# Performance work log

Hardware: AMD Instinct MI355X
Metric: run time of the kernel (lower is better)

The kernel has to match this reference:

```python
import jax, jax.numpy as jnp
import numpy as np

B, H, S, D = 2, 16, 2048, 64

def setup_inputs() -> dict:
    key = jax.random.key(0)
    kq, kk, kv, km = jax.random.split(key, 4)
    Query = jax.random.normal(kq, (B, H, S, D), dtype=jnp.float32)
    Key = jax.random.normal(kk, (B, H, S, D), dtype=jnp.float32)
    Value = jax.random.normal(kv, (B, H, S, D), dtype=jnp.float32)
    attention_mask = jax.random.randint(km, (B, 1, S, S), 0, 2).astype(jnp.bool_)
    return {"Query": Query, "Key": Key, "Value": Value,
            "attention_mask": attention_mask, "dim_key": D}

def reference(Query, Key, Value, attention_mask, dim_key):
    # scores: [B,H,S,S]
    scale = 1.0 / np.sqrt(dim_key).astype(np.float32)
    scores = jnp.einsum('bhqd,bhkd->bhqk', Query, Key) * scale
    scores = jnp.where(attention_mask, jnp.float32(-1e9), scores)
    attention = jax.nn.softmax(scores, axis=-1)
    context = jnp.einsum('bhqk,bhkd->bhqd', attention, Value)
    return (context, attention)
```

## Files before the change

### kernel.cpp

```cpp
#include <hip/hip_runtime.h>
#include <hip/hip_bf16.h>


#define S_LEN 2048
#define D_DIM 64
#define LOG2E 1.44269504088896340736f

typedef __attribute__((ext_vector_type(8))) short bf16x8;
typedef __attribute__((ext_vector_type(4))) float f32x4;

__device__ __forceinline__ short f2bs(float f) {
    union { __hip_bfloat16 h; short s; } u;
    u.h = __float2bfloat16(f);
    return u.s;
}

__device__ __forceinline__ unsigned int f2bs2(float x, float y) {
    float2 t = make_float2(x, y);
    union { __hip_bfloat162 h; unsigned int u; } u;
    u.h = __float22bfloat162_rn(t);
    return u.u;
}

__device__ __forceinline__ bf16x8 cvt8(float4 a, float4 b) {
    union { bf16x8 v; unsigned int w[4]; } u;
    u.w[0] = f2bs2(a.x, a.y);
    u.w[1] = f2bs2(a.z, a.w);
    u.w[2] = f2bs2(b.x, b.y);
    u.w[3] = f2bs2(b.z, b.w);
    return u.v;
}

__global__ __launch_bounds__(512, 4) void sdpa_kernel(
    const float* __restrict__ Q, const float* __restrict__ K,
    const float* __restrict__ V, const int* __restrict__ Mask,
    float* __restrict__ Ctx, float* __restrict__ Attn)
{
    __shared__ __attribute__((aligned(16))) short Kt[64 * 72];
    __shared__ __attribute__((aligned(16))) short Vt[64 * 72];
    __shared__ __attribute__((aligned(16))) short Pt[8 * 16 * 72];

    const int tid  = threadIdx.x;
    const int wave = tid >> 6;
    const int lane = tid & 63;
    const int quad = lane >> 4;
    const int l16  = lane & 15;

    const int bid = blockIdx.x;
    const int bh  = bid >> 4;
    const int qt  = bid & 15;
    const int b   = bh >> 4;

    const size_t sd_off = (size_t)bh * S_LEN * D_DIM;
    const float* Qbh = Q + sd_off;
    const float* Kbh = K + sd_off;
    const float* Vbh = V + sd_off;
    const int*   Mb  = Mask + (size_t)b * S_LEN * S_LEN;
    float* Cbh = Ctx + sd_off;
    float* Abh = Attn + (size_t)bh * S_LEN * S_LEN;

    const int qw = qt * 128 + wave * 16;

    bf16x8 qfrag[2];
    {
        const int qrow = qw + l16;
        #pragma unroll
        for (int kc = 0; kc < 2; ++kc) {
            const float* qp = Qbh + (size_t)qrow * D_DIM + kc * 32 + quad * 8;
            float4 a = *(const float4*)qp;
            float4 c = *(const float4*)(qp + 4);
            a.x *= 0.125f; a.y *= 0.125f; a.z *= 0.125f; a.w *= 0.125f;
            c.x *= 0.125f; c.y *= 0.125f; c.z *= 0.125f; c.w *= 0.125f;
            qfrag[kc] = cvt8(a, c);
        }
    }

    const int skey = tid >> 3;
    const int sd   = (tid & 7) * 8;

    float lacc[4] = {0.f, 0.f, 0.f, 0.f};

    for (int kt = 0; kt < 32; ++kt) {
        const int k0 = kt * 64;
        __syncthreads();
        {
            const float* kp = Kbh + (size_t)(k0 + skey) * D_DIM + sd;
            float4 a = *(const float4*)kp;
            float4 c = *(const float4*)(kp + 4);
            *(bf16x8*)&Kt[skey * 72 + sd] = cvt8(a, c);
        }
        __syncthreads();

        #pragma unroll
        for (int cc = 0; cc < 4; ++cc) {
            f32x4 acc = {0.f, 0.f, 0.f, 0.f};
            const int keyl = cc * 16 + l16;
            bf16x8 b0 = *(const bf16x8*)&Kt[keyl * 72 + quad * 8];
            bf16x8 b1 = *(const bf16x8*)&Kt[keyl * 72 + 32 + quad * 8];
            acc = __builtin_amdgcn_mfma_f32_16x16x32_bf16(qfrag[0], b0, acc, 0, 0, 0);
            acc = __builtin_amdgcn_mfma_f32_16x16x32_bf16(qfrag[1], b1, acc, 0, 0, 0);
            const int col = k0 + keyl;
            const int* mp = Mb + (size_t)(qw + quad * 4) * S_LEN + col;
            #pragma unroll
            for (int r = 0; r < 4; ++r) {
                int m = mp[(size_t)r * S_LEN];
                float p = m ? 0.f : exp2f(acc[r] * LOG2E);
                lacc[r] += p;
            }
        }
    }

    #pragma unroll
    for (int off = 1; off < 16; off <<= 1) {
        #pragma unroll
        for (int r = 0; r < 4; ++r)
            lacc[r] += __shfl_xor(lacc[r], off, 64);
    }
    float inv_l[4];
    #pragma unroll
    for (int r = 0; r < 4; ++r) inv_l[r] = 1.0f / lacc[r];

    f32x4 cacc[4];
    #pragma unroll
    for (int dc = 0; dc < 4; ++dc) cacc[dc] = (f32x4){0.f, 0.f, 0.f, 0.f};
    short* Pw = &Pt[wave * 16 * 72];

    for (int kt = 0; kt < 32; ++kt) {
        const int k0 = kt * 64;
        __syncthreads();
        {
            const float* kp = Kbh + (size_t)(k0 + skey) * D_DIM + sd;
            float4 a = *(const float4*)kp;
            float4 c = *(const float4*)(kp + 4);
            *(bf16x8*)&Kt[skey * 72 + sd] = cvt8(a, c);
            const float* vp = Vbh + (size_t)(k0 + skey) * D_DIM + sd;
            float4 va = *(const float4*)vp;
            float4 vb = *(const float4*)(vp + 4);
            float vv[8] = {va.x, va.y, va.z, va.w, vb.x, vb.y, vb.z, vb.w};
            #pragma unroll
            for (int i = 0; i < 8; ++i)
                Vt[(sd + i) * 72 + skey] = f2bs(vv[i]);
        }
        __syncthreads();

        #pragma unroll
        for (int cc = 0; cc < 4; ++cc) {
            f32x4 acc = {0.f, 0.f, 0.f, 0.f};
            const int keyl = cc * 16 + l16;
            bf16x8 b0 = *(const bf16x8*)&Kt[keyl * 72 + quad * 8];
            bf16x8 b1 = *(const bf16x8*)&Kt[keyl * 72 + 32 + quad * 8];
            acc = __builtin_amdgcn_mfma_f32_16x16x32_bf16(qfrag[0], b0, acc, 0, 0, 0);
            acc = __builtin_amdgcn_mfma_f32_16x16x32_bf16(qfrag[1], b1, acc, 0, 0, 0);
            const int col = k0 + keyl;
            const int* mp = Mb + (size_t)(qw + quad * 4) * S_LEN + col;
            float* ap = Abh + (size_t)(qw + quad * 4) * S_LEN + col;
            #pragma unroll
            for (int r = 0; r < 4; ++r) {
                int m = mp[(size_t)r * S_LEN];
                float p = m ? 0.f : exp2f(acc[r] * LOG2E);
                __builtin_nontemporal_store(p * inv_l[r], ap + (size_t)r * S_LEN);
                Pw[(quad * 4 + r) * 72 + keyl] = f2bs(p);
            }
        }

        #pragma unroll
        for (int kc = 0; kc < 2; ++kc) {
            bf16x8 af = *(const bf16x8*)&Pw[l16 * 72 + kc * 32 + quad * 8];
            #pragma unroll
            for (int dc = 0; dc < 4; ++dc) {
                bf16x8 bf = *(const bf16x8*)&Vt[(dc * 16 + l16) * 72 + kc * 32 + quad * 8];
                cacc[dc] = __builtin_amdgcn_mfma_f32_16x16x32_bf16(af, bf, cacc[dc], 0, 0, 0);
            }
        }
    }

    #pragma unroll
    for (int dc = 0; dc < 4; ++dc) {
        #pragma unroll
        for (int r = 0; r < 4; ++r) {
            Cbh[(size_t)(qw + quad * 4 + r) * D_DIM + dc * 16 + l16] =
                cacc[dc][r] * inv_l[r];
        }
    }
}

extern "C" void kernel_launch(void* const* d_in, const int* in_sizes, int n_in,
                              void* d_out, int out_size, void* d_ws, size_t ws_size,
                              hipStream_t stream) {
    const float* Q    = (const float*)d_in[0];
    const float* K    = (const float*)d_in[1];
    const float* V    = (const float*)d_in[2];
    const int*   Mask = (const int*)d_in[3];

    float* Ctx  = (float*)d_out;
    float* Attn = (float*)d_out + (size_t)2 * 16 * 2048 * 64;

    sdpa_kernel<<<dim3(512), dim3(512), 0, stream>>>(Q, K, V, Mask, Ctx, Attn);
}
```

Measured before the change: 760.8 us.

## Pre-convert K/V to bf16, bit-pack mask, use direct global-to-LDS loads

Adds a prep kernel that converts K and V to bf16 once, writing V pre-transposed, plus a kernel that packs the int mask into 64-bit bitmasks with ballot. The main kernel then loads tiles with global_load_lds into XOR-swizzled LDS, folds log2e into the Q scale, and uses native exp2. It also switches to 256-thread blocks of 64 queries with a head-grouped block order. This removes repeated per-block fp32 K/V conversion and the heavy int mask reads, in exchange for two extra launches and workspace traffic.

```diff
diff --git a/kernel.cpp b/kernel.cpp
--- a/kernel.cpp
+++ b/kernel.cpp
@@ -8,37 +8,93 @@
 
 typedef __attribute__((ext_vector_type(8))) short bf16x8;
 typedef __attribute__((ext_vector_type(4))) float f32x4;
-
+typedef unsigned long long u64;
+
+__device__ __forceinline__ unsigned int f2bs2(float x, float y) {
+    union { __hip_bfloat162 h; unsigned int u; } u;
+    u.h = __float22bfloat162_rn(make_float2(x, y));
+    return u.u;
+}
 __device__ __forceinline__ short f2bs(float f) {
     union { __hip_bfloat16 h; short s; } u;
     u.h = __float2bfloat16(f);
     return u.s;
 }
-
-__device__ __forceinline__ unsigned int f2bs2(float x, float y) {
-    float2 t = make_float2(x, y);
-    union { __hip_bfloat162 h; unsigned int u; } u;
-    u.h = __float22bfloat162_rn(t);
-    return u.u;
-}
-
 __device__ __forceinline__ bf16x8 cvt8(float4 a, float4 b) {
     union { bf16x8 v; unsigned int w[4]; } u;
-    u.w[0] = f2bs2(a.x, a.y);
-    u.w[1] = f2bs2(a.z, a.w);
-    u.w[2] = f2bs2(b.x, b.y);
-    u.w[3] = f2bs2(b.z, b.w);
+    u.w[0] = f2bs2(a.x, a.y); u.w[1] = f2bs2(a.z, a.w);
+    u.w[2] = f2bs2(b.x, b.y); u.w[3] = f2bs2(b.z, b.w);
     return u.v;
 }
 
-__global__ __launch_bounds__(512, 4) void sdpa_kernel(
-    const float* __restrict__ Q, const float* __restrict__ K,
-    const float* __restrict__ V, const int* __restrict__ Mask,
+__device__ __forceinline__ void gl2lds16(const short* g, short* l) {
+    __builtin_amdgcn_global_load_lds(
+        (const __attribute__((address_space(1))) unsigned int*)g,
+        (__attribute__((address_space(3))) unsigned int*)l, 16, 0, 0);
+}
+
+__global__ __launch_bounds__(256) void prep_kv(const float* __restrict__ K,
+                                               const float* __restrict__ V,
+                                               short* __restrict__ Kb,
+                                               short* __restrict__ Vtb) {
+    __shared__ short T[64 * 80];
+    const int bh = blockIdx.x >> 5;
+    const int kt = blockIdx.x & 31;
+    const int k0 = kt * 64;
+    const int t  = threadIdx.x;
+    const int row = t >> 2;
+    const int cq  = (t & 3) * 16;
+
+    const size_t base = (size_t)bh * S_LEN * D_DIM;
+    {
+        const float* kp = K + base + (size_t)(k0 + row) * D_DIM + cq;
+        float4 a = ((const float4*)kp)[0], b = ((const float4*)kp)[1],
+               c = ((const float4*)kp)[2], d = ((const float4*)kp)[3];
+        short* op = Kb + base + (size_t)(k0 + row) * D_DIM + cq;
+        *(bf16x8*)op       = cvt8(a, b);
+        *(bf16x8*)(op + 8) = cvt8(c, d);
+    }
+    {
+        const float* vp = V + base + (size_t)(k0 + row) * D_DIM + cq;
+        float4 a = ((const float4*)vp)[0], b = ((const float4*)vp)[1],
+               c = ((const float4*)vp)[2], d = ((const float4*)vp)[3];
+        float vv[16] = {a.x,a.y,a.z,a.w, b.x,b.y,b.z,b.w,
+                        c.x,c.y,c.z,c.w, d.x,d.y,d.z,d.w};
+        #pragma unroll
+        for (int i = 0; i < 16; ++i)
+            T[(cq + i) * 80 + row] = f2bs(vv[i]);
+    }
+    __syncthreads();
+    {
+        const int d  = t >> 2;
+        const int kc = (t & 3) * 16;
+        short* op = Vtb + (size_t)bh * D_DIM * S_LEN + (size_t)d * S_LEN + k0 + kc;
+        *(bf16x8*)op       = *(const bf16x8*)&T[d * 80 + kc];
+        *(bf16x8*)(op + 8) = *(const bf16x8*)&T[d * 80 + kc + 8];
+    }
+}
+
+__global__ __launch_bounds__(256) void mask_pack(const int* __restrict__ M,
+                                                 u64* __restrict__ Mp) {
+    const int lane = threadIdx.x & 63;
+    const int wid  = (blockIdx.x * 256 + threadIdx.x) >> 6;
+    const int nwaves = gridDim.x * 4;
+    const int nwords = 2 * S_LEN * (S_LEN / 64);
+    for (int w = wid; w < nwords; w += nwaves) {
+        int v = M[(size_t)w * 64 + lane];
+        u64 bits = __ballot(v != 0);
+        if (lane == 0) Mp[w] = bits;
+    }
+}
+
+__global__ __launch_bounds__(256, 4) void sdpa_main(
+    const float* __restrict__ Q, const short* __restrict__ Kb,
+    const short* __restrict__ Vtb, const u64* __restrict__ Mp,
     float* __restrict__ Ctx, float* __restrict__ Attn)
 {
-    __shared__ __attribute__((aligned(16))) short Kt[64 * 72];
-    __shared__ __attribute__((aligned(16))) short Vt[64 * 72];
-    __shared__ __attribute__((aligned(16))) short Pt[8 * 16 * 72];
+    __shared__ short Kt[64 * 64];
+    __shared__ short Vt[64 * 64];
+    __shared__ short Pt[4 * 16 * 80];
 
     const int tid  = threadIdx.x;
     const int wave = tid >> 6;
@@ -47,74 +103,68 @@
     const int l16  = lane & 15;
 
     const int bid = blockIdx.x;
-    const int bh  = bid >> 4;
-    const int qt  = bid & 15;
+    const int bh  = ((bid >> 8) << 3) | (bid & 7);
+    const int qt  = (bid >> 3) & 31;
     const int b   = bh >> 4;
+    const int qw  = qt * 64 + wave * 16;
 
     const size_t sd_off = (size_t)bh * S_LEN * D_DIM;
     const float* Qbh = Q + sd_off;
-    const float* Kbh = K + sd_off;
-    const float* Vbh = V + sd_off;
-    const int*   Mb  = Mask + (size_t)b * S_LEN * S_LEN;
+    const short* Kbh = Kb + sd_off;
+    const short* Vbh = Vtb + (size_t)bh * D_DIM * S_LEN;
     float* Cbh = Ctx + sd_off;
     float* Abh = Attn + (size_t)bh * S_LEN * S_LEN;
 
-    const int qw = qt * 128 + wave * 16;
-
     bf16x8 qfrag[2];
     {
         const int qrow = qw + l16;
+        const float s = 0.125f * LOG2E;
         #pragma unroll
         for (int kc = 0; kc < 2; ++kc) {
             const float* qp = Qbh + (size_t)qrow * D_DIM + kc * 32 + quad * 8;
-            float4 a = *(const float4*)qp;
-            float4 c = *(const float4*)(qp + 4);
-            a.x *= 0.125f; a.y *= 0.125f; a.z *= 0.125f; a.w *= 0.125f;
-            c.x *= 0.125f; c.y *= 0.125f; c.z *= 0.125f; c.w *= 0.125f;
+            float4 a = ((const float4*)qp)[0], c = ((const float4*)qp)[1];
+            a.x*=s; a.y*=s; a.z*=s; a.w*=s; c.x*=s; c.y*=s; c.z*=s; c.w*=s;
             qfrag[kc] = cvt8(a, c);
         }
     }
 
-    const int skey = tid >> 3;
-    const int sd   = (tid & 7) * 8;
+    const int mrow0 = (b * S_LEN + qw + quad * 4) * (S_LEN / 64);
 
     float lacc[4] = {0.f, 0.f, 0.f, 0.f};
-
     for (int kt = 0; kt < 32; ++kt) {
         const int k0 = kt * 64;
         __syncthreads();
-        {
-            const float* kp = Kbh + (size_t)(k0 + skey) * D_DIM + sd;
-            float4 a = *(const float4*)kp;
-            float4 c = *(const float4*)(kp + 4);
-            *(bf16x8*)&Kt[skey * 72 + sd] = cvt8(a, c);
-        }
-        __syncthreads();
-
+        #pragma unroll
+        for (int rd = 0; rd < 2; ++rd) {
+            const int m = tid + rd * 256;
+            const int row = m >> 3, sc = m & 7, c = sc ^ (row & 7);
+            gl2lds16(Kbh + (size_t)(k0 + row) * D_DIM + c * 8, &Kt[m * 8]);
+        }
+        __syncthreads();
+        u64 mw[4];
+        #pragma unroll
+        for (int r = 0; r < 4; ++r) mw[r] = Mp[mrow0 + r * 32 + kt];
         #pragma unroll
         for (int cc = 0; cc < 4; ++cc) {
+            const int keyl = cc * 16 + l16;
             f32x4 acc = {0.f, 0.f, 0.f, 0.f};
-            const int keyl = cc * 16 + l16;
-            bf16x8 b0 = *(const bf16x8*)&Kt[keyl * 72 + quad * 8];
-            bf16x8 b1 = *(const bf16x8*)&Kt[keyl * 72 + 32 + quad * 8];
-            acc = __builtin_amdgcn_mfma_f32_16x16x32_bf16(qfrag[0], b0, acc, 0, 0, 0);
-            acc = __builtin_amdgcn_mfma_f32_16x16x32_bf16(qfrag[1], b1, acc, 0, 0, 0);
-            const int col = k0 + keyl;
-            const int* mp = Mb + (size_t)(qw + quad * 4) * S_LEN + col;
+            #pragma unroll
+            for (int kc = 0; kc < 2; ++kc) {
+                bf16x8 bfr = *(const bf16x8*)&Kt[keyl * 64 + ((kc * 4 + quad) ^ (keyl & 7)) * 8];
+                acc = __builtin_amdgcn_mfma_f32_16x16x32_bf16(qfrag[kc], bfr, acc, 0, 0, 0);
+            }
             #pragma unroll
             for (int r = 0; r < 4; ++r) {
-                int m = mp[(size_t)r * S_LEN];
-                float p = m ? 0.f : exp2f(acc[r] * LOG2E);
+                float p = __builtin_amdgcn_exp2f(acc[r]);
+                p = ((mw[r] >> keyl) & 1ull) ? 0.f : p;
                 lacc[r] += p;
             }
         }
     }
-
     #pragma unroll
     for (int off = 1; off < 16; off <<= 1) {
         #pragma unroll
-        for (int r = 0; r < 4; ++r)
-            lacc[r] += __shfl_xor(lacc[r], off, 64);
+        for (int r = 0; r < 4; ++r) lacc[r] += __shfl_xor(lacc[r], off, 64);
     }
     float inv_l[4];
     #pragma unroll
@@ -123,53 +173,48 @@
     f32x4 cacc[4];
     #pragma unroll
     for (int dc = 0; dc < 4; ++dc) cacc[dc] = (f32x4){0.f, 0.f, 0.f, 0.f};
-    short* Pw = &Pt[wave * 16 * 72];
+    short* Pw = &Pt[wave * 16 * 80];
 
     for (int kt = 0; kt < 32; ++kt) {
         const int k0 = kt * 64;
         __syncthreads();
-        {
-            const float* kp = Kbh + (size_t)(k0 + skey) * D_DIM + sd;
-            float4 a = *(const float4*)kp;
-            float4 c = *(const float4*)(kp + 4);
-            *(bf16x8*)&Kt[skey * 72 + sd] = cvt8(a, c);
-            const float* vp = Vbh + (size_t)(k0 + skey) * D_DIM + sd;
-            float4 va = *(const float4*)vp;
-            float4 vb = *(const float4*)(vp + 4);
-            float vv[8] = {va.x, va.y, va.z, va.w, vb.x, vb.y, vb.z, vb.w};
-            #pragma unroll
-            for (int i = 0; i < 8; ++i)
-                Vt[(sd + i) * 72 + skey] = f2bs(vv[i]);
-        }
-        __syncthreads();
-
+        #pragma unroll
+        for (int rd = 0; rd < 2; ++rd) {
+            const int m = tid + rd * 256;
+            const int row = m >> 3, sc = m & 7, c = sc ^ (row & 7);
+            gl2lds16(Kbh + (size_t)(k0 + row) * D_DIM + c * 8, &Kt[m * 8]);
+            gl2lds16(Vbh + (size_t)row * S_LEN + k0 + c * 8, &Vt[m * 8]);
+        }
+        __syncthreads();
+        u64 mw[4];
+        #pragma unroll
+        for (int r = 0; r < 4; ++r) mw[r] = Mp[mrow0 + r * 32 + kt];
+        float* ap0 = Abh + (size_t)(qw + quad * 4) * S_LEN + k0;
         #pragma unroll
         for (int cc = 0; cc < 4; ++cc) {
+            const int keyl = cc * 16 + l16;
             f32x4 acc = {0.f, 0.f, 0.f, 0.f};
-            const int keyl = cc * 16 + l16;
-            bf16x8 b0 = *(const bf16x8*)&Kt[keyl * 72 + quad * 8];
-            bf16x8 b1 = *(const bf16x8*)&Kt[keyl * 72 + 32 + quad * 8];
-            acc = __builtin_amdgcn_mfma_f32_16x16x32_bf16(qfrag[0], b0, acc, 0, 0, 0);
-            acc = __builtin_amdgcn_mfma_f32_16x16x32_bf16(qfrag[1], b1, acc, 0, 0, 0);
-            const int col = k0 + keyl;
-            const int* mp = Mb + (size_t)(qw + quad * 4) * S_LEN + col;
-            float* ap = Abh + (size_t)(qw + quad * 4) * S_LEN + col;
+            #pragma unroll
+            for (int kc = 0; kc < 2; ++kc) {
+                bf16x8 bfr = *(const bf16x8*)&Kt[keyl * 64 + ((kc * 4 + quad) ^ (keyl & 7)) * 8];
+                acc = __builtin_amdgcn_mfma_f32_16x16x32_bf16(qfrag[kc], bfr, acc, 0, 0, 0);
+            }
             #pragma unroll
             for (int r = 0; r < 4; ++r) {
-                int m = mp[(size_t)r * S_LEN];
-                float p = m ? 0.f : exp2f(acc[r] * LOG2E);
-                __builtin_nontemporal_store(p * inv_l[r], ap + (size_t)r * S_LEN);
-                Pw[(quad * 4 + r) * 72 + keyl] = f2bs(p);
-            }
-        }
-
+                float p = __builtin_amdgcn_exp2f(acc[r]);
+                p = ((mw[r] >> keyl) & 1ull) ? 0.f : p;
+                __builtin_nontemporal_store(p * inv_l[r], ap0 + (size_t)r * S_LEN + keyl);
+                Pw[(quad * 4 + r) * 80 + keyl] = f2bs(p);
+            }
+        }
         #pragma unroll
         for (int kc = 0; kc < 2; ++kc) {
-            bf16x8 af = *(const bf16x8*)&Pw[l16 * 72 + kc * 32 + quad * 8];
+            bf16x8 af = *(const bf16x8*)&Pw[l16 * 80 + kc * 32 + quad * 8];
             #pragma unroll
             for (int dc = 0; dc < 4; ++dc) {
-                bf16x8 bf = *(const bf16x8*)&Vt[(dc * 16 + l16) * 72 + kc * 32 + quad * 8];
-                cacc[dc] = __builtin_amdgcn_mfma_f32_16x16x32_bf16(af, bf, cacc[dc], 0, 0, 0);
+                const int vrow = dc * 16 + l16;
+                bf16x8 bfr = *(const bf16x8*)&Vt[vrow * 64 + ((kc * 4 + quad) ^ (vrow & 7)) * 8];
+                cacc[dc] = __builtin_amdgcn_mfma_f32_16x16x32_bf16(af, bfr, cacc[dc], 0, 0, 0);
             }
         }
     }
@@ -195,5 +240,11 @@
     float* Ctx  = (float*)d_out;
     float* Attn = (float*)d_out + (size_t)2 * 16 * 2048 * 64;
 
-    sdpa_kernel<<<dim3(512), dim3(512), 0, stream>>>(Q, K, V, Mask, Ctx, Attn);
-}
+    short* Kb  = (short*)d_ws;
+    short* Vtb = (short*)((char*)d_ws + 8388608);
+    u64*   Mp  = (u64*)((char*)d_ws + 16777216);
+
+    prep_kv<<<dim3(1024), dim3(256), 0, stream>>>(K, V, Kb, Vtb);
+    mask_pack<<<dim3(512), dim3(256), 0, stream>>>(Mask, Mp);
+    sdpa_main<<<dim3(1024), dim3(256), 0, stream>>>(Q, Kb, Vtb, Mp, Ctx, Attn);
+}
```

Result: faster. 725.7 us (-4.6%).
